# Optimization experiments

Measured on AMD Instinct MI355X. Metric: run time of the kernel, lower is better.

## Reference

```python
import jax, jax.numpy as jnp
import numpy as np

HEADS = 8
BUCKETS = 64
TEMP = 0.75
SINKHORN_ITER = 5
EPS = 1e-6


def setup_inputs() -> dict:
    key = jax.random.key(0)
    ks = jax.random.split(key, 6)
    b, t, d = 2, 4096, 1024
    x = jax.random.normal(ks[0], (b, t, d), dtype=jnp.float32)
    gumbel_u = jax.random.uniform(ks[1], (b * HEADS, BUCKETS, BUCKETS), dtype=jnp.float32)
    w_qkv = jax.random.normal(ks[2], (d, 3 * d), dtype=jnp.float32) * (d ** -0.5)
    sort_w = jax.random.normal(ks[3], (1, HEADS, (d // HEADS) * 2, BUCKETS), dtype=jnp.float32)
    w_out = jax.random.normal(ks[4], (d, d), dtype=jnp.float32) * (d ** -0.5)
    b_out = jax.random.normal(ks[5], (d,), dtype=jnp.float32) * 0.01
    return {"x": x, "gumbel_u": gumbel_u, "w_qkv": w_qkv, "sort_w": sort_w,
            "w_out": w_out, "b_out": b_out}


def reference(x, gumbel_u, w_qkv, sort_w, w_out, b_out):
    b, t, d = x.shape
    h, buckets = HEADS, BUCKETS
    d_h = d // h
    bsz = t // buckets
    bh = b * h

    # qkv projection (no bias) and head merge -> (b*h, t, d_h)
    qkv = x @ w_qkv
    q, k, v = jnp.split(qkv, 3, axis=2)
    def merge_heads(u):
        return u.reshape(b, t, h, d_h).transpose(0, 2, 1, 3).reshape(bh, t, d_h)
    q, k, v = merge_heads(q), merge_heads(k), merge_heads(v)

    # bucket -> (bh, buckets, bsz, d_h)
    b_q = q.reshape(bh, buckets, bsz, d_h)
    b_k = k.reshape(bh, buckets, bsz, d_h)
    b_v = v.reshape(bh, buckets, bsz, d_h)

    # SortNet: bucket sums -> leaky_relu(x @ W), W per-head (2*d_h, buckets)
    sx = jnp.concatenate([b_q.sum(axis=2), b_k.sum(axis=2)], axis=-1)  # (bh, buckets, 2*d_h)
    W = jnp.broadcast_to(sort_w, (b, h, 2 * d_h, buckets)).reshape(bh, 2 * d_h, buckets)
    R = jax.nn.leaky_relu(jnp.einsum('bue,bec->buc', sx, W), negative_slope=0.01)

    # gumbel-sinkhorn (log clamped for finiteness; matches torch when R >= 0)
    g = -jnp.log(-jnp.log(gumbel_u + EPS) + EPS)
    r = (jnp.log(jnp.maximum(R + EPS, EPS)) + g) / TEMP
    for _ in range(SINKHORN_ITER):
        r = r - jax.nn.logsumexp(r, axis=2, keepdims=True)
        r = r - jax.nn.logsumexp(r, axis=1, keepdims=True)
    R = jnp.exp(r)

    # zero all but top-1 along last dim
    idx = jnp.argmax(R, axis=2)
    R = jnp.where(jnp.arange(buckets)[None, None, :] == idx[..., None], R, 0.0)

    # soft-permute buckets of k and v, concat with locals -> (bh, buckets, 2*bsz, d_h)
    k_r = jnp.einsum('buv,bvtd->butd', R, b_k)
    v_r = jnp.einsum('buv,bvtd->butd', R, b_v)
    b_k2 = jnp.concatenate([k_r, b_k], axis=2)
    b_v2 = jnp.concatenate([v_r, b_v], axis=2)

    # bucketed attention; NOTE: scale uses full model dim d (as in source)
    dots = jnp.einsum('buie,buje->buij', b_q, b_k2) * (d ** -0.5)
    attn = jax.nn.softmax(dots, axis=-1)
    out = jnp.einsum('buij,buje->buie', attn, b_v2)  # (bh, buckets, bsz, d_h)

    out = out.reshape(b, h, t, d_h).transpose(0, 2, 1, 3).reshape(b, t, d)
    return out @ w_out + b_out
```

## Files before the change

kernel.cpp:

```cpp
#include <hip/hip_runtime.h>
#include <stdint.h>

#define TEMP_ 0.75f
#define EPS_ 1e-6f

typedef __attribute__((ext_vector_type(8))) short bf16x8;
typedef __attribute__((ext_vector_type(4))) float f32x4;

typedef __attribute__((address_space(1))) void gvoid_t;
typedef __attribute__((address_space(3))) void lvoid_t;

__device__ __forceinline__ void async_ld16(const void* g, void* l) {
  __builtin_amdgcn_global_load_lds((gvoid_t*)g, (lvoid_t*)l, 16, 0, 0);
}

__device__ __forceinline__ float b2f(ushort u) {
  return __builtin_bit_cast(float, (uint32_t)u << 16);
}
__device__ __forceinline__ ushort f2b(float f) {
  uint32_t x = __builtin_bit_cast(uint32_t, f);
  x += 0x7fffu + ((x >> 16) & 1u);
  return (ushort)(x >> 16);
}

__device__ __forceinline__ uint32_t lds_u32(const void* p) {
  return (uint32_t)(uintptr_t)(lvoid_t*)p;
}

__device__ __forceinline__ bf16x8 dsr(uint32_t addr) {
  bf16x8 d;
  asm volatile("ds_read_b128 %0, %1" : "=v"(d) : "v"(addr));
  return d;
}

__global__ __launch_bounds__(256) void prep_x(
    const float* __restrict__ x, ushort* __restrict__ xb, float* __restrict__ xsum2) {
  const int blk = blockIdx.x;
  const int bu = blk >> 1, half = blk & 1;
  const int b = bu >> 6, u = bu & 63;
  const int c = threadIdx.x * 4;
  const float* src = x + ((size_t)(b * 4096 + u * 64 + half * 32)) * 1024 + c;
  ushort* dst = xb + ((size_t)(b * 4096 + u * 64 + half * 32)) * 1024 + c;
  float s0 = 0.f, s1 = 0.f, s2 = 0.f, s3 = 0.f;
  for (int pos = 0; pos < 32; pos++) {
    float4 v = *(const float4*)(src + (size_t)pos * 1024);
    s0 += v.x; s1 += v.y; s2 += v.z; s3 += v.w;
    ushort4 o;
    o.x = f2b(v.x); o.y = f2b(v.y); o.z = f2b(v.z); o.w = f2b(v.w);
    *(ushort4*)(dst + (size_t)pos * 1024) = o;
  }
  float4 sv = {s0, s1, s2, s3};
  *(float4*)&xsum2[(size_t)blk * 1024 + c] = sv;
}

__global__ __launch_bounds__(256) void transpose_f2b(
    const float* __restrict__ src, ushort* __restrict__ dst, int R, int C) {
  __shared__ float tile[32][33];
  int bx = blockIdx.x * 32;
  int by = blockIdx.y * 32;
  int tx = threadIdx.x & 31, ty = threadIdx.x >> 5;
  #pragma unroll
  for (int i = 0; i < 32; i += 8)
    tile[ty + i][tx] = src[(size_t)(by + ty + i) * C + bx + tx];
  __syncthreads();
  #pragma unroll
  for (int i = 0; i < 32; i += 8)
    dst[(size_t)(bx + ty + i) * R + by + tx] = f2b(tile[tx][ty + i]);
}

__global__ __launch_bounds__(256) void sx_gemm_partial(
    const float* __restrict__ xsum2, const float* __restrict__ wqkv,
    float* __restrict__ SXP) {
  __shared__ float xs[128 * 8];
  const int cb = blockIdx.x;
  const int rt = blockIdx.y;
  const int kc = blockIdx.z;
  const int tid = threadIdx.x;
  for (int idx = tid; idx < 1024; idx += 256) {
    int k = idx >> 3, r = idx & 7;
    int bu = rt * 8 + r;
    int kk = kc * 128 + k;
    xs[idx] = xsum2[(size_t)(bu * 2) * 1024 + kk] + xsum2[(size_t)(bu * 2 + 1) * 1024 + kk];
  }
  __syncthreads();
  const int n = cb * 256 + tid;
  float acc[8];
  #pragma unroll
  for (int r = 0; r < 8; r++) acc[r] = 0.f;
  for (int k = 0; k < 128; k++) {
    float w = wqkv[(size_t)(kc * 128 + k) * 3072 + n];
    float4 a0 = *(const float4*)&xs[k * 8];
    float4 a1 = *(const float4*)&xs[k * 8 + 4];
    acc[0] += a0.x * w; acc[1] += a0.y * w; acc[2] += a0.z * w; acc[3] += a0.w * w;
    acc[4] += a1.x * w; acc[5] += a1.y * w; acc[6] += a1.z * w; acc[7] += a1.w * w;
  }
  #pragma unroll
  for (int r = 0; r < 8; r++)
    SXP[(size_t)(kc * 128 + rt * 8 + r) * 2048 + n] = acc[r];
}

__global__ __launch_bounds__(256) void sx_reduce(
    const float* __restrict__ SXP, float* __restrict__ SX) {
  const int bu = blockIdx.y;
  const int n = blockIdx.x * 256 + threadIdx.x;
  float s = 0.f;
  #pragma unroll
  for (int kc = 0; kc < 8; kc++)
    s += SXP[(size_t)(kc * 128 + bu) * 2048 + n];
  const int head = (n >> 7) & 7;
  const int e2 = ((n >> 10) << 7) | (n & 127);
  const int b = bu >> 6, u = bu & 63;
  SX[((size_t)((b * 8 + head) * 256) + e2) * 64 + u] = s;
}

__global__ __launch_bounds__(256) void sortnet_sinkhorn(
    const float* __restrict__ SX, const float* __restrict__ sortw,
    const float* __restrict__ gum, int* __restrict__ idxArr,
    float* __restrict__ wgtArr) {
  __shared__ float sxl[64 * 64];
  __shared__ float wl[64 * 64];
  __shared__ float rr[64 * 65];
  __shared__ float redA[256];
  __shared__ float redB[256];
  __shared__ int redi[256];
  const int bh = blockIdx.x, tid = threadIdx.x, head = bh & 7;
  const int ui = tid & 15, ci = tid >> 4;

  float acc[4][4];
  #pragma unroll
  for (int i = 0; i < 4; i++)
    #pragma unroll
    for (int j = 0; j < 4; j++) acc[i][j] = 0.f;

  const f32x4* SX4 = (const f32x4*)(SX + (size_t)bh * 16384);
  const f32x4* W4 = (const f32x4*)(sortw + (size_t)head * 16384);
  f32x4* sxl4 = (f32x4*)sxl;
  f32x4* wl4 = (f32x4*)wl;

  #pragma unroll 1
  for (int ch = 0; ch < 4; ch++) {
    __syncthreads();
    #pragma unroll 1
    for (int g = tid; g < 1024; g += 256) {
      sxl4[g] = SX4[ch * 1024 + g];
      wl4[g] = W4[ch * 1024 + g];
    }
    __syncthreads();
    #pragma unroll 2
    for (int e = 0; e < 64; e++) {
      f32x4 a = sxl4[e * 16 + ui];
      f32x4 w = wl4[e * 16 + ci];
      #pragma unroll
      for (int i = 0; i < 4; i++)
        #pragma unroll
        for (int j = 0; j < 4; j++) acc[i][j] += a[i] * w[j];
    }
  }

  #pragma unroll
  for (int i = 0; i < 4; i++)
    #pragma unroll
    for (int j = 0; j < 4; j++) {
      int u = ui * 4 + i, c = ci * 4 + j;
      float dot = acc[i][j];
      float r0 = dot > 0.f ? dot : 0.01f * dot;
      float gu = gum[(size_t)bh * 4096 + u * 64 + c];
      float inner = -logf(gu + EPS_) + EPS_;
      float g = -logf(fmaxf(inner, 1e-38f));
      rr[u * 65 + c] = (logf(fmaxf(r0 + EPS_, EPS_)) + g) / TEMP_;
    }
  __syncthreads();

  const int su = tid & 63, sq = tid >> 6;
  #pragma unroll 1
  for (int it = 0; it < 5; it++) {
    {
      float pm = -1e30f;
      #pragma unroll
      for (int j = 0; j < 16; j++) pm = fmaxf(pm, rr[su * 65 + sq * 16 + j]);
      redA[sq * 64 + su] = pm;
      __syncthreads();
      float m = fmaxf(fmaxf(redA[su], redA[64 + su]), fmaxf(redA[128 + su], redA[192 + su]));
      float ps = 0.f;
      #pragma unroll
      for (int j = 0; j < 16; j++) ps += expf(rr[su * 65 + sq * 16 + j] - m);
      redB[sq * 64 + su] = ps;
      __syncthreads();
      float l = m + logf(redB[su] + redB[64 + su] + redB[128 + su] + redB[192 + su]);
      #pragma unroll
      for (int j = 0; j < 16; j++) rr[su * 65 + sq * 16 + j] -= l;
      __syncthreads();
    }
    {
      float pm = -1e30f;
      #pragma unroll
      for (int j = 0; j < 16; j++) pm = fmaxf(pm, rr[(sq * 16 + j) * 65 + su]);
      redA[sq * 64 + su] = pm;
      __syncthreads();
      float m = fmaxf(fmaxf(redA[su], redA[64 + su]), fmaxf(redA[128 + su], redA[192 + su]));
      float ps = 0.f;
      #pragma unroll
      for (int j = 0; j < 16; j++) ps += expf(rr[(sq * 16 + j) * 65 + su] - m);
      redB[sq * 64 + su] = ps;
      __syncthreads();
      float l = m + logf(redB[su] + redB[64 + su] + redB[128 + su] + redB[192 + su]);
      #pragma unroll
      for (int j = 0; j < 16; j++) rr[(sq * 16 + j) * 65 + su] -= l;
      __syncthreads();
    }
  }

  {
    float pv = -1e30f;
    int pi = 0;
    #pragma unroll
    for (int j = 0; j < 16; j++) {
      float v = rr[su * 65 + sq * 16 + j];
      if (v > pv) { pv = v; pi = sq * 16 + j; }
    }
    redA[sq * 64 + su] = pv;
    redi[sq * 64 + su] = pi;
    __syncthreads();
    if (tid < 64) {
      float best = -1e30f;
      int bi = 0;
      #pragma unroll
      for (int q = 0; q < 4; q++) {
        float v = redA[q * 64 + tid];
        if (v > best) { best = v; bi = redi[q * 64 + tid]; }
      }
      idxArr[bh * 64 + tid] = bi;
      wgtArr[bh * 64 + tid] = expf(fminf(best, 80.f));
    }
  }
}

__global__ __launch_bounds__(256, 2) void gemm_bt(
    const ushort* __restrict__ A, const ushort* __restrict__ BT,
    int M, int N, int K, int mode,
    const float* __restrict__ bias, float* __restrict__ Cout,
    ushort* __restrict__ Qb, ushort* __restrict__ Kb, ushort* __restrict__ VT) {
  __shared__ ushort As[2][128 * 64];
  __shared__ ushort Bs[2][128 * 64];
  const int tid = threadIdx.x;
  const int wave = tid >> 6, lane = tid & 63;
  const int quad = lane >> 4, l16 = lane & 15;
  const int m0 = blockIdx.y * 128, n0 = blockIdx.x * 128;
  const int wm = (wave >> 1) * 64, wn = (wave & 1) * 64;
  const ushort* Ap = A + (uint64_t)m0 * K;
  const ushort* Bp = BT + (uint64_t)n0 * K;

  auto stage = [&](const ushort* G, int k0, ushort* buf) {
    #pragma unroll
    for (int q = 0; q < 4; ++q) {
      int p = q * 256 + tid;
      int row = p >> 3, pp = p & 7;
      int cc = pp ^ (row & 7);
      async_ld16(G + (uint64_t)row * K + k0 + cc * 8,
                 buf + (q * 256 + wave * 64) * 8);
    }
  };

  const uint32_t asB = lds_u32(&As[0][0]);
  const uint32_t bsB = lds_u32(&Bs[0][0]);
  uint32_t aoff[2][4], boff[2][4];
  #pragma unroll
  for (int kk = 0; kk < 2; ++kk) {
    int pc = (kk * 4 + quad) ^ (l16 & 7);
    #pragma unroll
    for (int mt = 0; mt < 4; ++mt) {
      aoff[kk][mt] = (uint32_t)((wm + mt * 16 + l16) * 128 + pc * 16);
      boff[kk][mt] = (uint32_t)((wn + mt * 16 + l16) * 128 + pc * 16);
    }
  }

  f32x4 acc[4][4];
  #pragma unroll
  for (int i = 0; i < 4; i++)
    #pragma unroll
    for (int j = 0; j < 4; j++) acc[i][j] = (f32x4){0.f, 0.f, 0.f, 0.f};

  const int NT = K >> 6;
  stage(Ap, 0, As[0]);
  stage(Bp, 0, Bs[0]);
  stage(Ap, 64, As[1]);
  stage(Bp, 64, Bs[1]);

  #pragma unroll 1
  for (int t = 0; t < NT; ++t) {
    if (t < NT - 1)
      asm volatile("s_waitcnt vmcnt(8)\n\ts_barrier" ::: "memory");
    else
      asm volatile("s_waitcnt vmcnt(0)\n\ts_barrier" ::: "memory");

    const uint32_t ab = asB + (uint32_t)(t & 1) * 16384u;
    const uint32_t bb = bsB + (uint32_t)(t & 1) * 16384u;
    bf16x8 a[2][4], b[2][4];
    #pragma unroll
    for (int kk = 0; kk < 2; ++kk) {
      #pragma unroll
      for (int mt = 0; mt < 4; ++mt) a[kk][mt] = dsr(ab + aoff[kk][mt]);
      #pragma unroll
      for (int nt = 0; nt < 4; ++nt) b[kk][nt] = dsr(bb + boff[kk][nt]);
    }
    asm volatile("s_waitcnt lgkmcnt(0)" ::: "memory");
    __builtin_amdgcn_sched_barrier(0);
    __builtin_amdgcn_s_setprio(1);
    #pragma unroll
    for (int kk = 0; kk < 2; ++kk)
      #pragma unroll
      for (int mt = 0; mt < 4; ++mt)
        #pragma unroll
        for (int nt = 0; nt < 4; ++nt)
          acc[mt][nt] = __builtin_amdgcn_mfma_f32_16x16x32_bf16(a[kk][mt], b[kk][nt], acc[mt][nt], 0, 0, 0);
    __builtin_amdgcn_s_setprio(0);
    asm volatile("s_barrier" ::: "memory");
    if (t + 2 < NT) {
      stage(Ap, (t + 2) * 64, As[t & 1]);
      stage(Bp, (t + 2) * 64, Bs[t & 1]);
    }
  }

  if (mode == 0) {
    #pragma unroll
    for (int mt = 0; mt < 4; mt++) {
      int row = m0 + wm + mt * 16 + quad * 4;
      #pragma unroll
      for (int nt = 0; nt < 4; nt++) {
        int col = n0 + wn + nt * 16 + l16;
        float bv = bias[col];
        #pragma unroll
        for (int r = 0; r < 4; r++)
          Cout[(uint64_t)(row + r) * N + col] = acc[mt][nt][r] + bv;
      }
    }
  } else {
    int which = blockIdx.x >> 3;
    int head = blockIdx.x & 7;
    #pragma unroll
    for (int mt = 0; mt < 4; mt++) {
      int mrow = m0 + wm + mt * 16 + quad * 4;
      int bidx = mrow >> 12;
      int ttok = mrow & 4095;
      int u = ttok >> 6, pos = ttok & 63;
      int bh = bidx * 8 + head;
      #pragma unroll
      for (int nt = 0; nt < 4; nt++) {
        int e = wn + nt * 16 + l16;
        if (which == 2) {
          ushort4 pk;
          pk.x = f2b(acc[mt][nt][0]);
          pk.y = f2b(acc[mt][nt][1]);
          pk.z = f2b(acc[mt][nt][2]);
          pk.w = f2b(acc[mt][nt][3]);
          *(ushort4*)&VT[((uint64_t)(bh * 64 + u) * 128 + e) * 64 + pos] = pk;
        } else {
          ushort* dst = (which == 0) ? Qb : Kb;
          #pragma unroll
          for (int r = 0; r < 4; r++)
            dst[((uint64_t)(bh * 64 + u) * 64 + pos + r) * 128 + e] = f2b(acc[mt][nt][r]);
        }
      }
    }
  }
}

#define KSTR 136
__global__ __launch_bounds__(256) void attn_kernel(
    const ushort* __restrict__ Qb, const ushort* __restrict__ Kb,
    const ushort* __restrict__ VT, const int* __restrict__ idxArr,
    const float* __restrict__ wgtArr, ushort* __restrict__ attn_out) {
  __shared__ ushort Qs[64 * KSTR];
  __shared__ ushort Ks[128 * KSTR];
  const int blk = blockIdx.x;
  const int u = blk & 63, bh = blk >> 6;
  const int tid = threadIdx.x, wave = tid >> 6, lane = tid & 63;
  const int quad = lane >> 4, l16 = lane & 15;
  const int vu = idxArr[bh * 64 + u] & 63;
  const float w = wgtArr[bh * 64 + u];

  const ushort* Qsrc = Qb + (uint64_t)(bh * 64 + u) * 8192;
  const ushort* Ksrc0 = Kb + (uint64_t)(bh * 64 + vu) * 8192;
  const ushort* Ksrc1 = Kb + (uint64_t)(bh * 64 + u) * 8192;
  const ushort* Vsrc0 = VT + (uint64_t)(bh * 64 + vu) * 8192;
  const ushort* Vsrc1 = VT + (uint64_t)(bh * 64 + u) * 8192;

  for (int g = tid; g < 64 * 16; g += 256) {
    int eb = g & 15, p = g >> 4;
    *(bf16x8*)&Qs[p * KSTR + eb * 8] = *(const bf16x8*)&Qsrc[p * 128 + eb * 8];
  }
  for (int g = tid; g < 128 * 16; g += 256) {
    int eb = g & 15, j = g >> 4;
    const ushort* s = (j < 64) ? &Ksrc0[j * 128 + eb * 8] : &Ksrc1[(j - 64) * 128 + eb * 8];
    *(bf16x8*)&Ks[j * KSTR + eb * 8] = *(const bf16x8*)s;
  }
  __syncthreads();

  f32x4 S[8];
  #pragma unroll
  for (int nt = 0; nt < 8; nt++) S[nt] = (f32x4){0.f, 0.f, 0.f, 0.f};
  #pragma unroll
  for (int kk = 0; kk < 4; kk++) {
    bf16x8 aq = *(const bf16x8*)&Qs[(wave * 16 + l16) * KSTR + kk * 32 + quad * 8];
    #pragma unroll
    for (int nt = 0; nt < 8; nt++) {
      bf16x8 bk = *(const bf16x8*)&Ks[(nt * 16 + l16) * KSTR + kk * 32 + quad * 8];
      S[nt] = __builtin_amdgcn_mfma_f32_16x16x32_bf16(aq, bk, S[nt], 0, 0, 0);
    }
  }
  __syncthreads();

  for (int g = tid; g < 128 * 16; g += 256) {
    int jb = g & 15, e = g >> 4;
    const ushort* s = (jb < 8) ? &Vsrc0[e * 64 + jb * 8] : &Vsrc1[e * 64 + (jb - 8) * 8];
    *(bf16x8*)&Ks[e * KSTR + jb * 8] = *(const bf16x8*)s;
  }

  const float scale = 0.03125f;
  float rowmax[4] = {-1e30f, -1e30f, -1e30f, -1e30f};
  #pragma unroll
  for (int nt = 0; nt < 8; nt++) {
    float cs = scale * ((nt < 4) ? w : 1.0f);
    #pragma unroll
    for (int r = 0; r < 4; r++) {
      S[nt][r] *= cs;
      rowmax[r] = fmaxf(rowmax[r], S[nt][r]);
    }
  }
  #pragma unroll
  for (int off = 1; off < 16; off <<= 1)
    #pragma unroll
    for (int r = 0; r < 4; r++)
      rowmax[r] = fmaxf(rowmax[r], __shfl_xor(rowmax[r], off, 64));
  float rowsum[4] = {0.f, 0.f, 0.f, 0.f};
  #pragma unroll
  for (int nt = 0; nt < 8; nt++)
    #pragma unroll
    for (int r = 0; r < 4; r++) {
      float p = expf(S[nt][r] - rowmax[r]);
      S[nt][r] = p;
      rowsum[r] += p;
    }
  #pragma unroll
  for (int off = 1; off < 16; off <<= 1)
    #pragma unroll
    for (int r = 0; r < 4; r++)
      rowsum[r] += __shfl_xor(rowsum[r], off, 64);
  float rinv[4];
  #pragma unroll
  for (int r = 0; r < 4; r++) rinv[r] = 1.0f / rowsum[r];

  #pragma unroll
  for (int nt = 0; nt < 8; nt++)
    #pragma unroll
    for (int r = 0; r < 4; r++) {
      float pv = S[nt][r] * rinv[r] * ((nt < 4) ? w : 1.0f);
      Qs[(wave * 16 + quad * 4 + r) * KSTR + nt * 16 + l16] = f2b(pv);
    }
  __syncthreads();

  f32x4 O[8];
  #pragma unroll
  for (int nt = 0; nt < 8; nt++) O[nt] = (f32x4){0.f, 0.f, 0.f, 0.f};
  #pragma unroll
  for (int kk = 0; kk < 4; kk++) {
    bf16x8 ap = *(const bf16x8*)&Qs[(wave * 16 + l16) * KSTR + kk * 32 + quad * 8];
    #pragma unroll
    for (int nt = 0; nt < 8; nt++) {
      bf16x8 bv = *(const bf16x8*)&Ks[(nt * 16 + l16) * KSTR + kk * 32 + quad * 8];
      O[nt] = __builtin_amdgcn_mfma_f32_16x16x32_bf16(ap, bv, O[nt], 0, 0, 0);
    }
  }

  const int bidx = bh >> 3, head = bh & 7;
  uint64_t rowbase =
      (uint64_t)(bidx * 4096 + u * 64 + wave * 16 + quad * 4) * 1024 + head * 128;
  #pragma unroll
  for (int nt = 0; nt < 8; nt++)
    #pragma unroll
    for (int r = 0; r < 4; r++)
      attn_out[rowbase + (uint64_t)r * 1024 + nt * 16 + l16] = f2b(O[nt][r]);
}

extern "C" void kernel_launch(void* const* d_in, const int* in_sizes, int n_in,
                              void* d_out, int out_size, void* d_ws, size_t ws_size,
                              hipStream_t stream) {
  (void)in_sizes; (void)n_in; (void)out_size; (void)ws_size;
  const float* x = (const float*)d_in[0];
  const float* gum = (const float*)d_in[1];
  const float* wqkv = (const float*)d_in[2];
  const float* sortw = (const float*)d_in[3];
  const float* wout = (const float*)d_in[4];
  const float* bout = (const float*)d_in[5];
  float* out = (float*)d_out;

  char* ws = (char*)d_ws;
  size_t off = 0;
  auto alloc = [&](size_t bytes) {
    char* p = ws + off;
    off += (bytes + 255) & ~(size_t)255;
    return p;
  };
  ushort* xb = (ushort*)alloc((size_t)8192 * 1024 * 2);
  float* xsum2 = (float*)alloc((size_t)256 * 1024 * 4);
  ushort* wqkvT = (ushort*)alloc((size_t)3072 * 1024 * 2);
  ushort* woutT = (ushort*)alloc((size_t)1024 * 1024 * 2);
  float* SX = (float*)alloc((size_t)16 * 256 * 64 * 4);
  ushort* Qb = (ushort*)alloc((size_t)16 * 64 * 64 * 128 * 2);
  ushort* Kb = (ushort*)alloc((size_t)16 * 64 * 64 * 128 * 2);
  ushort* VT = (ushort*)alloc((size_t)16 * 64 * 128 * 64 * 2);
  int* idxArr = (int*)alloc((size_t)16 * 64 * 4);
  float* wgtArr = (float*)alloc((size_t)16 * 64 * 4);
  ushort* attn = xb;
  float* SXP = (float*)Qb;

  prep_x<<<256, 256, 0, stream>>>(x, xb, xsum2);
  transpose_f2b<<<dim3(3072 / 32, 1024 / 32), 256, 0, stream>>>(wqkv, wqkvT, 1024, 3072);
  transpose_f2b<<<dim3(1024 / 32, 1024 / 32), 256, 0, stream>>>(wout, woutT, 1024, 1024);
  sx_gemm_partial<<<dim3(8, 16, 8), 256, 0, stream>>>(xsum2, wqkv, SXP);
  sx_reduce<<<dim3(8, 128), 256, 0, stream>>>(SXP, SX);
  sortnet_sinkhorn<<<16, 256, 0, stream>>>(SX, sortw, gum, idxArr, wgtArr);
  gemm_bt<<<dim3(3072 / 128, 8192 / 128), 256, 0, stream>>>(
      xb, wqkvT, 8192, 3072, 1024, 1, nullptr, nullptr, Qb, Kb, VT);
  attn_kernel<<<16 * 64, 256, 0, stream>>>(Qb, Kb, VT, idxArr, wgtArr, attn);
  gemm_bt<<<dim3(1024 / 128, 8192 / 128), 256, 0, stream>>>(
      attn, woutT, 8192, 1024, 1024, 0, bout, out, nullptr, nullptr, nullptr);
}
```

Before: 271.2 us.

## Fuse prep kernels, widen sx GEMM rows, swizzle GEMM blocks, split MFMA wait

Merges the x-conversion and both weight-transpose kernels into one launch to cut launch overhead and let the pieces run concurrently. The sx partial GEMM now handles 32 rows per block instead of 8, so each weight load is reused four times as often, at the cost of more registers. gemm_bt remaps block indices with a stride-8 swizzle, intended to improve L2 locality. It also issues the first half of the MFMAs once the first LDS reads have landed, overlapping LDS latency with compute.

Result: no change. 270.7 us (-0.2%).

```diff
diff --git a/kernel.cpp b/kernel.cpp
--- a/kernel.cpp
+++ b/kernel.cpp
@@ -33,32 +33,44 @@
   return d;
 }
 
-__global__ __launch_bounds__(256) void prep_x(
-    const float* __restrict__ x, ushort* __restrict__ xb, float* __restrict__ xsum2) {
+__global__ __launch_bounds__(256) void prep_fused(
+    const float* __restrict__ x, ushort* __restrict__ xb, float* __restrict__ xsum2,
+    const float* __restrict__ wqkv, ushort* __restrict__ wqkvT,
+    const float* __restrict__ wout, ushort* __restrict__ woutT) {
+  __shared__ float tile[32][33];
   const int blk = blockIdx.x;
-  const int bu = blk >> 1, half = blk & 1;
-  const int b = bu >> 6, u = bu & 63;
-  const int c = threadIdx.x * 4;
-  const float* src = x + ((size_t)(b * 4096 + u * 64 + half * 32)) * 1024 + c;
-  ushort* dst = xb + ((size_t)(b * 4096 + u * 64 + half * 32)) * 1024 + c;
-  float s0 = 0.f, s1 = 0.f, s2 = 0.f, s3 = 0.f;
-  for (int pos = 0; pos < 32; pos++) {
-    float4 v = *(const float4*)(src + (size_t)pos * 1024);
-    s0 += v.x; s1 += v.y; s2 += v.z; s3 += v.w;
-    ushort4 o;
-    o.x = f2b(v.x); o.y = f2b(v.y); o.z = f2b(v.z); o.w = f2b(v.w);
-    *(ushort4*)(dst + (size_t)pos * 1024) = o;
-  }
-  float4 sv = {s0, s1, s2, s3};
-  *(float4*)&xsum2[(size_t)blk * 1024 + c] = sv;
-}
-
-__global__ __launch_bounds__(256) void transpose_f2b(
-    const float* __restrict__ src, ushort* __restrict__ dst, int R, int C) {
-  __shared__ float tile[32][33];
-  int bx = blockIdx.x * 32;
-  int by = blockIdx.y * 32;
-  int tx = threadIdx.x & 31, ty = threadIdx.x >> 5;
+  const int tid = threadIdx.x;
+  if (blk < 256) {
+    const int bu = blk >> 1, half = blk & 1;
+    const int b = bu >> 6, u = bu & 63;
+    const int c = tid * 4;
+    const float* src = x + ((size_t)(b * 4096 + u * 64 + half * 32)) * 1024 + c;
+    ushort* dst = xb + ((size_t)(b * 4096 + u * 64 + half * 32)) * 1024 + c;
+    float s0 = 0.f, s1 = 0.f, s2 = 0.f, s3 = 0.f;
+    for (int pos = 0; pos < 32; pos++) {
+      float4 v = *(const float4*)(src + (size_t)pos * 1024);
+      s0 += v.x; s1 += v.y; s2 += v.z; s3 += v.w;
+      ushort4 o;
+      o.x = f2b(v.x); o.y = f2b(v.y); o.z = f2b(v.z); o.w = f2b(v.w);
+      *(ushort4*)(dst + (size_t)pos * 1024) = o;
+    }
+    float4 sv = {s0, s1, s2, s3};
+    *(float4*)&xsum2[(size_t)blk * 1024 + c] = sv;
+    return;
+  }
+  const float* src;
+  ushort* dst;
+  int R, C, bx, by;
+  if (blk < 256 + 3072) {
+    int lin = blk - 256;
+    src = wqkv; dst = wqkvT; R = 1024; C = 3072;
+    bx = (lin % 96) * 32; by = (lin / 96) * 32;
+  } else {
+    int lin = blk - 3328;
+    src = wout; dst = woutT; R = 1024; C = 1024;
+    bx = (lin % 32) * 32; by = (lin / 32) * 32;
+  }
+  int tx = tid & 31, ty = tid >> 5;
   #pragma unroll
   for (int i = 0; i < 32; i += 8)
     tile[ty + i][tx] = src[(size_t)(by + ty + i) * C + bx + tx];
@@ -71,32 +83,40 @@
 __global__ __launch_bounds__(256) void sx_gemm_partial(
     const float* __restrict__ xsum2, const float* __restrict__ wqkv,
     float* __restrict__ SXP) {
-  __shared__ float xs[128 * 8];
+  __shared__ float xs[128 * 36];
   const int cb = blockIdx.x;
   const int rt = blockIdx.y;
   const int kc = blockIdx.z;
   const int tid = threadIdx.x;
-  for (int idx = tid; idx < 1024; idx += 256) {
-    int k = idx >> 3, r = idx & 7;
-    int bu = rt * 8 + r;
+  #pragma unroll
+  for (int it = 0; it < 16; ++it) {
+    int idx = it * 256 + tid;
+    int k = idx & 127, r = idx >> 7;
+    int bu = rt * 32 + r;
     int kk = kc * 128 + k;
-    xs[idx] = xsum2[(size_t)(bu * 2) * 1024 + kk] + xsum2[(size_t)(bu * 2 + 1) * 1024 + kk];
+    xs[k * 36 + r] =
+        xsum2[(size_t)(bu * 2) * 1024 + kk] + xsum2[(size_t)(bu * 2 + 1) * 1024 + kk];
   }
   __syncthreads();
   const int n = cb * 256 + tid;
-  float acc[8];
-  #pragma unroll
-  for (int r = 0; r < 8; r++) acc[r] = 0.f;
+  float acc[32];
+  #pragma unroll
+  for (int r = 0; r < 32; r++) acc[r] = 0.f;
+  #pragma unroll 2
   for (int k = 0; k < 128; k++) {
     float w = wqkv[(size_t)(kc * 128 + k) * 3072 + n];
-    float4 a0 = *(const float4*)&xs[k * 8];
-    float4 a1 = *(const float4*)&xs[k * 8 + 4];
-    acc[0] += a0.x * w; acc[1] += a0.y * w; acc[2] += a0.z * w; acc[3] += a0.w * w;
-    acc[4] += a1.x * w; acc[5] += a1.y * w; acc[6] += a1.z * w; acc[7] += a1.w * w;
-  }
-  #pragma unroll
-  for (int r = 0; r < 8; r++)
-    SXP[(size_t)(kc * 128 + rt * 8 + r) * 2048 + n] = acc[r];
+    #pragma unroll
+    for (int j = 0; j < 8; ++j) {
+      f32x4 a = *(const f32x4*)&xs[k * 36 + j * 4];
+      acc[j * 4 + 0] += a[0] * w;
+      acc[j * 4 + 1] += a[1] * w;
+      acc[j * 4 + 2] += a[2] * w;
+      acc[j * 4 + 3] += a[3] * w;
+    }
+  }
+  #pragma unroll
+  for (int r = 0; r < 32; r++)
+    SXP[(size_t)(kc * 128 + rt * 32 + r) * 2048 + n] = acc[r];
 }
 
 __global__ __launch_bounds__(256) void sx_reduce(
@@ -245,7 +265,12 @@
   const int tid = threadIdx.x;
   const int wave = tid >> 6, lane = tid & 63;
   const int quad = lane >> 4, l16 = lane & 15;
-  const int m0 = blockIdx.y * 128, n0 = blockIdx.x * 128;
+  const int gx = gridDim.x;
+  const int lin = blockIdx.y * gx + blockIdx.x;
+  const int nwg = gx * gridDim.y;
+  const int swz = (lin & 7) * (nwg >> 3) + (lin >> 3);
+  const int bx = swz % gx, by = swz / gx;
+  const int m0 = by * 128, n0 = bx * 128;
   const int wm = (wave >> 1) * 64, wn = (wave & 1) * 64;
   const ushort* Ap = A + (uint64_t)m0 * K;
   const ushort* Bp = BT + (uint64_t)n0 * K;
@@ -303,16 +328,23 @@
       #pragma unroll
       for (int nt = 0; nt < 4; ++nt) b[kk][nt] = dsr(bb + boff[kk][nt]);
     }
+    asm volatile("s_waitcnt lgkmcnt(8)" ::: "memory");
+    __builtin_amdgcn_sched_barrier(0);
+    __builtin_amdgcn_s_setprio(1);
+    #pragma unroll
+    for (int mt = 0; mt < 4; ++mt)
+      #pragma unroll
+      for (int nt = 0; nt < 4; ++nt)
+        acc[mt][nt] = __builtin_amdgcn_mfma_f32_16x16x32_bf16(a[0][mt], b[0][nt], acc[mt][nt], 0, 0, 0);
+    __builtin_amdgcn_s_setprio(0);
     asm volatile("s_waitcnt lgkmcnt(0)" ::: "memory");
     __builtin_amdgcn_sched_barrier(0);
     __builtin_amdgcn_s_setprio(1);
     #pragma unroll
-    for (int kk = 0; kk < 2; ++kk)
-      #pragma unroll
-      for (int mt = 0; mt < 4; ++mt)
-        #pragma unroll
-        for (int nt = 0; nt < 4; ++nt)
-          acc[mt][nt] = __builtin_amdgcn_mfma_f32_16x16x32_bf16(a[kk][mt], b[kk][nt], acc[mt][nt], 0, 0, 0);
+    for (int mt = 0; mt < 4; ++mt)
+      #pragma unroll
+      for (int nt = 0; nt < 4; ++nt)
+        acc[mt][nt] = __builtin_amdgcn_mfma_f32_16x16x32_bf16(a[1][mt], b[1][nt], acc[mt][nt], 0, 0, 0);
     __builtin_amdgcn_s_setprio(0);
     asm volatile("s_barrier" ::: "memory");
     if (t + 2 < NT) {
@@ -335,8 +367,8 @@
       }
     }
   } else {
-    int which = blockIdx.x >> 3;
-    int head = blockIdx.x & 7;
+    int which = bx >> 3;
+    int head = bx & 7;
     #pragma unroll
     for (int mt = 0; mt < 4; mt++) {
       int mrow = m0 + wm + mt * 16 + quad * 4;
@@ -514,10 +546,8 @@
   ushort* attn = xb;
   float* SXP = (float*)Qb;
 
-  prep_x<<<256, 256, 0, stream>>>(x, xb, xsum2);
-  transpose_f2b<<<dim3(3072 / 32, 1024 / 32), 256, 0, stream>>>(wqkv, wqkvT, 1024, 3072);
-  transpose_f2b<<<dim3(1024 / 32, 1024 / 32), 256, 0, stream>>>(wout, woutT, 1024, 1024);
-  sx_gemm_partial<<<dim3(8, 16, 8), 256, 0, stream>>>(xsum2, wqkv, SXP);
+  prep_fused<<<4352, 256, 0, stream>>>(x, xb, xsum2, wqkv, wqkvT, wout, woutT);
+  sx_gemm_partial<<<dim3(8, 4, 8), 256, 0, stream>>>(xsum2, wqkv, SXP);
   sx_reduce<<<dim3(8, 128), 256, 0, stream>>>(SXP, SX);
   sortnet_sinkhorn<<<16, 256, 0, stream>>>(SX, sortw, gum, idxArr, wgtArr);
   gemm_bt<<<dim3(3072 / 128, 8192 / 128), 256, 0, stream>>>(
```

## Split GEMM into specialized QKV and output kernels with block swizzle and split LDS wait

Applied to the files above, without the earlier changes.

Splits the shared gemm_bt into gemm_qkv and gemm_out. gemm_qkv hardcodes K, remaps block indices with an 8-way swizzle meant to improve cache locality, and splits the LDS wait so the first half of the MFMAs starts before all fragment reads finish. gemm_out is a new, simpler single-buffered kernel with no cross-iteration prefetch, which adds exposed load latency for the output projection. The mode branch is removed from both kernels.

Result: faster. 265.6 us (-2.0%).

```diff
diff --git a/kernel.cpp b/kernel.cpp
--- a/kernel.cpp
+++ b/kernel.cpp
@@ -235,17 +235,21 @@
   }
 }
 
-__global__ __launch_bounds__(256, 2) void gemm_bt(
+__global__ __launch_bounds__(256, 2) void gemm_qkv(
     const ushort* __restrict__ A, const ushort* __restrict__ BT,
-    int M, int N, int K, int mode,
-    const float* __restrict__ bias, float* __restrict__ Cout,
     ushort* __restrict__ Qb, ushort* __restrict__ Kb, ushort* __restrict__ VT) {
+  const int K = 1024;
   __shared__ ushort As[2][128 * 64];
   __shared__ ushort Bs[2][128 * 64];
   const int tid = threadIdx.x;
   const int wave = tid >> 6, lane = tid & 63;
   const int quad = lane >> 4, l16 = lane & 15;
-  const int m0 = blockIdx.y * 128, n0 = blockIdx.x * 128;
+  const int gx = gridDim.x;
+  const int lin = blockIdx.y * gx + blockIdx.x;
+  const int nwg = gx * gridDim.y;
+  const int swz = (lin & 7) * (nwg >> 3) + (lin >> 3);
+  const int bx = swz % gx, by = swz / gx;
+  const int m0 = by * 128, n0 = bx * 128;
   const int wm = (wave >> 1) * 64, wn = (wave & 1) * 64;
   const ushort* Ap = A + (uint64_t)m0 * K;
   const ushort* Bp = BT + (uint64_t)n0 * K;
@@ -303,16 +307,23 @@
       #pragma unroll
       for (int nt = 0; nt < 4; ++nt) b[kk][nt] = dsr(bb + boff[kk][nt]);
     }
+    asm volatile("s_waitcnt lgkmcnt(8)" ::: "memory");
+    __builtin_amdgcn_sched_barrier(0);
+    __builtin_amdgcn_s_setprio(1);
+    #pragma unroll
+    for (int mt = 0; mt < 4; ++mt)
+      #pragma unroll
+      for (int nt = 0; nt < 4; ++nt)
+        acc[mt][nt] = __builtin_amdgcn_mfma_f32_16x16x32_bf16(a[0][mt], b[0][nt], acc[mt][nt], 0, 0, 0);
+    __builtin_amdgcn_s_setprio(0);
     asm volatile("s_waitcnt lgkmcnt(0)" ::: "memory");
     __builtin_amdgcn_sched_barrier(0);
     __builtin_amdgcn_s_setprio(1);
     #pragma unroll
-    for (int kk = 0; kk < 2; ++kk)
-      #pragma unroll
-      for (int mt = 0; mt < 4; ++mt)
-        #pragma unroll
-        for (int nt = 0; nt < 4; ++nt)
-          acc[mt][nt] = __builtin_amdgcn_mfma_f32_16x16x32_bf16(a[kk][mt], b[kk][nt], acc[mt][nt], 0, 0, 0);
+    for (int mt = 0; mt < 4; ++mt)
+      #pragma unroll
+      for (int nt = 0; nt < 4; ++nt)
+        acc[mt][nt] = __builtin_amdgcn_mfma_f32_16x16x32_bf16(a[1][mt], b[1][nt], acc[mt][nt], 0, 0, 0);
     __builtin_amdgcn_s_setprio(0);
     asm volatile("s_barrier" ::: "memory");
     if (t + 2 < NT) {
@@ -321,46 +332,103 @@
     }
   }
 
-  if (mode == 0) {
-    #pragma unroll
-    for (int mt = 0; mt < 4; mt++) {
-      int row = m0 + wm + mt * 16 + quad * 4;
-      #pragma unroll
-      for (int nt = 0; nt < 4; nt++) {
-        int col = n0 + wn + nt * 16 + l16;
-        float bv = bias[col];
+  int which = bx >> 3;
+  int head = bx & 7;
+  #pragma unroll
+  for (int mt = 0; mt < 4; mt++) {
+    int mrow = m0 + wm + mt * 16 + quad * 4;
+    int bidx = mrow >> 12;
+    int ttok = mrow & 4095;
+    int u = ttok >> 6, pos = ttok & 63;
+    int bh = bidx * 8 + head;
+    #pragma unroll
+    for (int nt = 0; nt < 4; nt++) {
+      int e = wn + nt * 16 + l16;
+      if (which == 2) {
+        ushort4 pk;
+        pk.x = f2b(acc[mt][nt][0]);
+        pk.y = f2b(acc[mt][nt][1]);
+        pk.z = f2b(acc[mt][nt][2]);
+        pk.w = f2b(acc[mt][nt][3]);
+        *(ushort4*)&VT[((uint64_t)(bh * 64 + u) * 128 + e) * 64 + pos] = pk;
+      } else {
+        ushort* dst = (which == 0) ? Qb : Kb;
         #pragma unroll
         for (int r = 0; r < 4; r++)
-          Cout[(uint64_t)(row + r) * N + col] = acc[mt][nt][r] + bv;
+          dst[((uint64_t)(bh * 64 + u) * 64 + pos + r) * 128 + e] = f2b(acc[mt][nt][r]);
       }
     }
-  } else {
-    int which = blockIdx.x >> 3;
-    int head = blockIdx.x & 7;
-    #pragma unroll
-    for (int mt = 0; mt < 4; mt++) {
-      int mrow = m0 + wm + mt * 16 + quad * 4;
-      int bidx = mrow >> 12;
-      int ttok = mrow & 4095;
-      int u = ttok >> 6, pos = ttok & 63;
-      int bh = bidx * 8 + head;
-      #pragma unroll
-      for (int nt = 0; nt < 4; nt++) {
-        int e = wn + nt * 16 + l16;
-        if (which == 2) {
-          ushort4 pk;
-          pk.x = f2b(acc[mt][nt][0]);
-          pk.y = f2b(acc[mt][nt][1]);
-          pk.z = f2b(acc[mt][nt][2]);
-          pk.w = f2b(acc[mt][nt][3]);
-          *(ushort4*)&VT[((uint64_t)(bh * 64 + u) * 128 + e) * 64 + pos] = pk;
-        } else {
-          ushort* dst = (which == 0) ? Qb : Kb;
-          #pragma unroll
-          for (int r = 0; r < 4; r++)
-            dst[((uint64_t)(bh * 64 + u) * 64 + pos + r) * 128 + e] = f2b(acc[mt][nt][r]);
-        }
-      }
+  }
+}
+
+__global__ __launch_bounds__(256, 2) void gemm_out(
+    const ushort* __restrict__ A, const ushort* __restrict__ BT,
+    int M, int N, int K,
+    const float* __restrict__ bias, float* __restrict__ Cout) {
+  __shared__ ushort As_lo[128 * 32];
+  __shared__ ushort As_hi[128 * 32];
+  __shared__ ushort Bs_lo[128 * 32];
+  __shared__ ushort Bs_hi[128 * 32];
+  const int tid = threadIdx.x;
+  const int wave = tid >> 6, lane = tid & 63;
+  const int quad = lane >> 4, l16 = lane & 15;
+  const int m0 = blockIdx.y * 128, n0 = blockIdx.x * 128;
+  const int wm = (wave >> 1) * 64, wn = (wave & 1) * 64;
+
+  f32x4 acc[4][4];
+  #pragma unroll
+  for (int i = 0; i < 4; i++)
+    #pragma unroll
+    for (int j = 0; j < 4; j++) acc[i][j] = (f32x4){0.f, 0.f, 0.f, 0.f};
+
+  const int srow = wave * 32 + (lane >> 2);
+  const int schunk = (lane & 3) * 8;
+
+  for (int k0 = 0; k0 < K; k0 += 64) {
+    __syncthreads();
+    {
+      const ushort* gA0 = A + (uint64_t)(m0 + srow) * K + k0 + schunk;
+      const ushort* gB0 = BT + (uint64_t)(n0 + srow) * K + k0 + schunk;
+      const int lofs = (wave * 32) * 32;
+      async_ld16(gA0, (ushort*)As_lo + lofs);
+      async_ld16(gA0 + (uint64_t)16 * K, (ushort*)As_lo + lofs + 16 * 32);
+      async_ld16(gA0 + 32, (ushort*)As_hi + lofs);
+      async_ld16(gA0 + (uint64_t)16 * K + 32, (ushort*)As_hi + lofs + 16 * 32);
+      async_ld16(gB0, (ushort*)Bs_lo + lofs);
+      async_ld16(gB0 + (uint64_t)16 * K, (ushort*)Bs_lo + lofs + 16 * 32);
+      async_ld16(gB0 + 32, (ushort*)Bs_hi + lofs);
+      async_ld16(gB0 + (uint64_t)16 * K + 32, (ushort*)Bs_hi + lofs + 16 * 32);
+    }
+    __syncthreads();
+    #pragma unroll
+    for (int kk = 0; kk < 2; kk++) {
+      const ushort* Ab = kk ? As_hi : As_lo;
+      const ushort* Bb = kk ? Bs_hi : Bs_lo;
+      bf16x8 af[4], bfr[4];
+      #pragma unroll
+      for (int mt = 0; mt < 4; mt++)
+        af[mt] = *(const bf16x8*)&Ab[(wm + mt * 16 + l16) * 32 + quad * 8];
+      #pragma unroll
+      for (int nt = 0; nt < 4; nt++)
+        bfr[nt] = *(const bf16x8*)&Bb[(wn + nt * 16 + l16) * 32 + quad * 8];
+      #pragma unroll
+      for (int mt = 0; mt < 4; mt++)
+        #pragma unroll
+        for (int nt = 0; nt < 4; nt++)
+          acc[mt][nt] = __builtin_amdgcn_mfma_f32_16x16x32_bf16(af[mt], bfr[nt], acc[mt][nt], 0, 0, 0);
+    }
+  }
+
+  #pragma unroll
+  for (int mt = 0; mt < 4; mt++) {
+    int row = m0 + wm + mt * 16 + quad * 4;
+    #pragma unroll
+    for (int nt = 0; nt < 4; nt++) {
+      int col = n0 + wn + nt * 16 + l16;
+      float bv = bias[col];
+      #pragma unroll
+      for (int r = 0; r < 4; r++)
+        Cout[(uint64_t)(row + r) * N + col] = acc[mt][nt][r] + bv;
     }
   }
 }
@@ -520,9 +588,8 @@
   sx_gemm_partial<<<dim3(8, 16, 8), 256, 0, stream>>>(xsum2, wqkv, SXP);
   sx_reduce<<<dim3(8, 128), 256, 0, stream>>>(SXP, SX);
   sortnet_sinkhorn<<<16, 256, 0, stream>>>(SX, sortw, gum, idxArr, wgtArr);
-  gemm_bt<<<dim3(3072 / 128, 8192 / 128), 256, 0, stream>>>(
-      xb, wqkvT, 8192, 3072, 1024, 1, nullptr, nullptr, Qb, Kb, VT);
+  gemm_qkv<<<dim3(3072 / 128, 8192 / 128), 256, 0, stream>>>(xb, wqkvT, Qb, Kb, VT);
   attn_kernel<<<16 * 64, 256, 0, stream>>>(Qb, Kb, VT, idxArr, wgtArr, attn);
-  gemm_bt<<<dim3(1024 / 128, 8192 / 128), 256, 0, stream>>>(
-      attn, woutT, 8192, 1024, 1024, 0, bout, out, nullptr, nullptr, nullptr);
-}
+  gemm_out<<<dim3(1024 / 128, 8192 / 128), 256, 0, stream>>>(
+      attn, woutT, 8192, 1024, 1024, bout, out);
+}
```
